# Kernel tuning notes

Measured on AMD Instinct MI355X. Metric: run time of the kernel, lower is better.

Reference implementation:

```python
import jax, jax.numpy as jnp
import numpy as np

N = 100000
E = 3200000
IN_C, H1, H2 = 512, 64, 32


def gcn_norm(edge_index, edge_weight, num_nodes):
    """PyG gcn_norm with add_self_loops=True: D^-1/2 (A+I) D^-1/2 edge weights."""
    row, col = edge_index[0], edge_index[1]
    loop = jnp.arange(num_nodes, dtype=edge_index.dtype)
    row = jnp.concatenate([row, loop])
    col = jnp.concatenate([col, loop])
    w = jnp.concatenate([edge_weight, jnp.ones((num_nodes,), edge_weight.dtype)])
    deg = jax.ops.segment_sum(w, col, num_segments=num_nodes)
    dinv = jnp.where(deg > 0, jax.lax.rsqrt(jnp.maximum(deg, 1e-12)), 0.0)
    wnorm = dinv[row] * w * dinv[col]
    return row, col, wnorm


def gcn_conv(x, W, b, row, col, wnorm, num_nodes):
    h = x @ W                                   # [N, out] linear first (out <= in)
    msg = wnorm[:, None] * h[row]               # gather + per-edge scale  [E+N, out]
    out = jax.ops.segment_sum(msg, col, num_segments=num_nodes)
    return out + b


def setup_inputs() -> dict:
    key = jax.random.key(0)
    ks = jax.random.split(key, 9)
    x = jax.random.normal(ks[0], (N, IN_C), dtype=jnp.float32)
    edge_index = jax.random.randint(ks[1], (2, E), 0, N, dtype=jnp.int64)
    edge_weight = jax.random.uniform(ks[2], (E,), dtype=jnp.float32)
    # Glorot-style init for GCN linear weights, zero bias (PyG defaults).
    def glorot(k, fan_in, fan_out):
        s = np.sqrt(6.0 / (fan_in + fan_out)).astype(np.float32)
        return jax.random.uniform(k, (fan_in, fan_out), jnp.float32, -s, s)
    return {
        "x": x,
        "edge_index": edge_index,
        "edge_weight": edge_weight,
        "W1": glorot(ks[3], IN_C, H1), "b1": jnp.zeros((H1,), jnp.float32),
        "W2": glorot(ks[4], H1, H2),  "b2": jnp.zeros((H2,), jnp.float32),
        "W3": glorot(ks[5], H2, 1),   "b3": jnp.zeros((1,), jnp.float32),
    }


def reference(x, edge_index, edge_weight, W1, b1, W2, b2, W3, b3):
    # Inference mode: dropout is identity (training=False).
    row, col, wnorm = gcn_norm(edge_index, edge_weight, N)  # cached=True: shared across layers
    h = jax.nn.relu(gcn_conv(x, W1, b1, row, col, wnorm, N))
    h = jax.nn.relu(gcn_conv(h, W2, b2, row, col, wnorm, N))
    h = gcn_conv(h, W3, b3, row, col, wnorm, N)
    return h.reshape(-1)  # [N]
```

## Files before the change

kernel.cpp:

```cpp
#include <hip/hip_runtime.h>

constexpr int BLK = 256;
constexpr int NBLKBIN = 512;
constexpr int MAXNB   = 1024;

typedef __bf16 bf16x8 __attribute__((ext_vector_type(8)));
typedef float  f32x4  __attribute__((ext_vector_type(4)));

__device__ __forceinline__ float blo(unsigned u) { return __uint_as_float(u << 16); }
__device__ __forceinline__ float bhi(unsigned u) { return __uint_as_float(u & 0xffff0000u); }

__global__ void k_detect(const int* __restrict__ ei, int e, int* __restrict__ flag) {
    if (blockIdx.x == 0 && threadIdx.x == 0) {
        int is64 = 1;
        for (int i = 0; i < 16; ++i)
            if (ei[2 * i + 1] != 0) { is64 = 0; break; }
        *flag = is64;
    }
}

__device__ __forceinline__ int load_idx(const void* ei, size_t pos, int is64) {
    if (is64) return (int)((const long long*)ei)[pos];
    return ((const int*)ei)[pos];
}

__global__ void k_zero_i(int* __restrict__ p, int n) {
    long i = (long)blockIdx.x * BLK + threadIdx.x;
    if (i < n) p[i] = 0;
}

__global__ __launch_bounds__(256) void k_binhist(const void* __restrict__ ei, int e,
                                                 const int* __restrict__ flag,
                                                 int* __restrict__ bucket_cnt, int nb) {
    __shared__ int hist[MAXNB];
    const int t = threadIdx.x;
    for (int b = t; b < nb; b += 256) hist[b] = 0;
    __syncthreads();
    const int is64 = *flag;
    const int chunk = (e + NBLKBIN - 1) / NBLKBIN;
    const int i0 = blockIdx.x * chunk;
    const int i1 = min(e, i0 + chunk);
    for (int i = i0 + t; i < i1; i += 256) {
        int dst = load_idx(ei, (size_t)e + i, is64);
        atomicAdd(&hist[dst >> 7], 1);
    }
    __syncthreads();
    for (int b = t; b < nb; b += 256) {
        int c = hist[b];
        if (c) atomicAdd(&bucket_cnt[b], c);
    }
}

__global__ void k_scanbkt(const int* __restrict__ cnt, int* __restrict__ offs,
                          int* __restrict__ cursor, int nb, int e) {
    __shared__ int sh[256];
    const int t = threadIdx.x;
    const int base = t * 4;
    int v[4]; int s = 0;
#pragma unroll
    for (int k = 0; k < 4; ++k) {
        int i = base + k;
        v[k] = (i < nb) ? cnt[i] : 0;
        s += v[k];
    }
    sh[t] = s;
    __syncthreads();
    for (int d = 1; d < 256; d <<= 1) {
        int x = (t >= d) ? sh[t - d] : 0;
        __syncthreads();
        sh[t] += x;
        __syncthreads();
    }
    int excl = (t == 0) ? 0 : sh[t - 1];
#pragma unroll
    for (int k = 0; k < 4; ++k) {
        int i = base + k;
        if (i < nb) { offs[i] = excl; cursor[i] = excl; excl += v[k]; }
    }
    if (t == 255) offs[nb] = e;
}

__global__ __launch_bounds__(256) void k_binscatter(const void* __restrict__ ei,
                                                    const float* __restrict__ ew, int e,
                                                    const int* __restrict__ flag,
                                                    int* __restrict__ bucket_cursor,
                                                    int2* __restrict__ binned, int nb) {
    __shared__ int hist[MAXNB];
    const int t = threadIdx.x;
    for (int b = t; b < nb; b += 256) hist[b] = 0;
    __syncthreads();
    const int is64 = *flag;
    const int chunk = (e + NBLKBIN - 1) / NBLKBIN;
    const int i0 = blockIdx.x * chunk;
    const int i1 = min(e, i0 + chunk);
    for (int i = i0 + t; i < i1; i += 256) {
        int dst = load_idx(ei, (size_t)e + i, is64);
        atomicAdd(&hist[dst >> 7], 1);
    }
    __syncthreads();
    for (int b = t; b < nb; b += 256) {
        int c = hist[b];
        int base = 0;
        if (c) base = atomicAdd(&bucket_cursor[b], c);
        hist[b] = base;
    }
    __syncthreads();
    for (int i = i0 + t; i < i1; i += 256) {
        int dst = load_idx(ei, (size_t)e + i, is64);
        int src = load_idx(ei, (size_t)i, is64);
        float w = ew[i];
        int bin = dst >> 7;
        int pos = atomicAdd(&hist[bin], 1);
        binned[pos] = make_int2(src | ((dst & 127) << 20), __float_as_int(w));
    }
}

__global__ __launch_bounds__(256) void k_bucketcnt(const int* __restrict__ bucket_offs,
                                                   const int2* __restrict__ binned,
                                                   int* __restrict__ counts,
                                                   float* __restrict__ dinv, int n) {
    __shared__ int   icnt[128];
    __shared__ float facc[128];
    const int t = threadIdx.x;
    const int k = blockIdx.x;
    if (t < 128) { icnt[t] = 0; facc[t] = 0.f; }
    __syncthreads();
    const int j0 = bucket_offs[k], j1 = bucket_offs[k + 1];
    for (int j = j0 + t; j < j1; j += 256) {
        int2 p = binned[j];
        int dl = ((unsigned)p.x) >> 20;
        atomicAdd(&icnt[dl], 1);
        atomicAdd(&facc[dl], __int_as_float(p.y));
    }
    __syncthreads();
    if (t < 128) {
        int nd = k * 128 + t;
        if (nd < n) {
            counts[nd] = icnt[t];
            dinv[nd] = rsqrtf(1.0f + facc[t]);
        }
    }
}

__global__ void k_scan1(const int* __restrict__ in, int* __restrict__ out,
                        int* __restrict__ bsum, int n) {
    __shared__ int sh[256];
    const int t = threadIdx.x;
    const int base = blockIdx.x * 1024 + t * 4;
    int v[4];
    int s = 0;
#pragma unroll
    for (int k = 0; k < 4; ++k) {
        int i = base + k;
        v[k] = (i < n) ? in[i] : 0;
        s += v[k];
    }
    sh[t] = s;
    __syncthreads();
    for (int d = 1; d < 256; d <<= 1) {
        int x = (t >= d) ? sh[t - d] : 0;
        __syncthreads();
        sh[t] += x;
        __syncthreads();
    }
    int excl = (t == 0) ? 0 : sh[t - 1];
    if (t == 255) bsum[blockIdx.x] = sh[255];
#pragma unroll
    for (int k = 0; k < 4; ++k) {
        int i = base + k;
        if (i < n) { out[i] = excl; excl += v[k]; }
    }
}

__global__ void k_scan2(int* __restrict__ bsum, int nb) {
    __shared__ int sh[128];
    const int t = threadIdx.x;
    sh[t] = (t < nb) ? bsum[t] : 0;
    __syncthreads();
    for (int d = 1; d < 128; d <<= 1) {
        int x = (t >= d) ? sh[t - d] : 0;
        __syncthreads();
        sh[t] += x;
        __syncthreads();
    }
    if (t < nb) bsum[t] = (t == 0) ? 0 : sh[t - 1];
}

__global__ void k_scan3(int* __restrict__ offs, const int* __restrict__ scanned,
                        const int* __restrict__ bsum, int n, int e) {
    long i = (long)blockIdx.x * BLK + threadIdx.x;
    if (i < n) offs[i] = scanned[i] + bsum[i >> 10];
    if (i == 0) offs[n] = e;
}

__global__ __launch_bounds__(256) void k_place(const int* __restrict__ bucket_offs,
                                               const int2* __restrict__ binned,
                                               const int* __restrict__ offs,
                                               const float* __restrict__ dinv,
                                               int2* __restrict__ csrp, int n) {
    __shared__ int cur[128];
    const int t = threadIdx.x;
    const int k = blockIdx.x;
    if (t < 128) {
        int nd = k * 128 + t;
        cur[t] = (nd < n) ? offs[nd] : 0;
    }
    __syncthreads();
    const int j0 = bucket_offs[k], j1 = bucket_offs[k + 1];
    for (int j = j0 + t; j < j1; j += 256) {
        int2 p = binned[j];
        int dl  = ((unsigned)p.x) >> 20;
        int src = p.x & 0xFFFFF;
        int pos = atomicAdd(&cur[dl], 1);
        float w2 = __int_as_float(p.y) * dinv[src];
        csrp[pos] = make_int2(src, __float_as_int(w2));
    }
}

__global__ void k_wcvt_frag(const float* __restrict__ W, __bf16* __restrict__ Wtf) {
    int i = blockIdx.x * BLK + threadIdx.x;
    if (i >= 4096) return;
    int lane = i & 63;
    int t    = (i >> 6) & 3;
    int k0c  = i >> 8;
    int col  = t * 16 + (lane & 15);
    int kbase = k0c * 32 + (lane >> 4) * 8;
    bf16x8 v;
#pragma unroll
    for (int j = 0; j < 8; ++j) v[j] = (__bf16)W[(size_t)(kbase + j) * 64 + col];
    *(bf16x8*)(Wtf + (size_t)i * 8) = v;
}

__global__ void k_wcvt_frag2(const float* __restrict__ W, __bf16* __restrict__ Wtf2) {
    int i = threadIdx.x;
    int lane = i & 63;
    int ct   = i >> 6;
    int t = ct & 1, chunk = ct >> 1;
    int col  = t * 16 + (lane & 15);
    int kbase = chunk * 32 + (lane >> 4) * 8;
    bf16x8 v;
#pragma unroll
    for (int j = 0; j < 8; ++j) v[j] = (__bf16)W[(size_t)(kbase + j) * 32 + col];
    *(bf16x8*)(Wtf2 + (size_t)i * 8) = v;
}

__global__ __launch_bounds__(256) void k_gemm1_mfma(const float* __restrict__ X,
                                                    const __bf16* __restrict__ Wtf,
                                                    __bf16* __restrict__ H, int nrows) {
    const int wave = threadIdx.x >> 6;
    const int lane = threadIdx.x & 63;
    const int l15  = lane & 15;
    const int lq   = lane >> 4;
    const long rbase = (long)blockIdx.x * 128 + wave * 32;

    long ar0 = rbase + l15;      if (ar0 >= nrows) ar0 = nrows - 1;
    long ar1 = rbase + 16 + l15; if (ar1 >= nrows) ar1 = nrows - 1;
    const float4* x0 = (const float4*)(X + (size_t)ar0 * 512) + lq * 2;
    const float4* x1 = (const float4*)(X + (size_t)ar1 * 512) + lq * 2;

    f32x4 acc[2][4];
#pragma unroll
    for (int r = 0; r < 2; ++r)
#pragma unroll
        for (int t = 0; t < 4; ++t) acc[r][t] = f32x4{0.f, 0.f, 0.f, 0.f};

    float4 pa[2][2][2];
#pragma unroll
    for (int s = 0; s < 2; ++s) {
        pa[s][0][0] = x0[s * 8]; pa[s][0][1] = x0[s * 8 + 1];
        pa[s][1][0] = x1[s * 8]; pa[s][1][1] = x1[s * 8 + 1];
    }

#pragma unroll
    for (int k0c = 0; k0c < 16; ++k0c) {
        const int s = k0c & 1;
        float4 a00 = pa[s][0][0], a01 = pa[s][0][1];
        float4 a10 = pa[s][1][0], a11 = pa[s][1][1];
        if (k0c + 2 < 16) {
            pa[s][0][0] = x0[(k0c + 2) * 8]; pa[s][0][1] = x0[(k0c + 2) * 8 + 1];
            pa[s][1][0] = x1[(k0c + 2) * 8]; pa[s][1][1] = x1[(k0c + 2) * 8 + 1];
        }
        bf16x8 af0, af1;
        af0[0] = (__bf16)a00.x; af0[1] = (__bf16)a00.y; af0[2] = (__bf16)a00.z; af0[3] = (__bf16)a00.w;
        af0[4] = (__bf16)a01.x; af0[5] = (__bf16)a01.y; af0[6] = (__bf16)a01.z; af0[7] = (__bf16)a01.w;
        af1[0] = (__bf16)a10.x; af1[1] = (__bf16)a10.y; af1[2] = (__bf16)a10.z; af1[3] = (__bf16)a10.w;
        af1[4] = (__bf16)a11.x; af1[5] = (__bf16)a11.y; af1[6] = (__bf16)a11.z; af1[7] = (__bf16)a11.w;
#pragma unroll
        for (int t = 0; t < 4; ++t) {
            bf16x8 bf_ = *(const bf16x8*)(Wtf + ((size_t)(k0c * 4 + t) * 64 + lane) * 8);
            acc[0][t] = __builtin_amdgcn_mfma_f32_16x16x32_bf16(af0, bf_, acc[0][t], 0, 0, 0);
            acc[1][t] = __builtin_amdgcn_mfma_f32_16x16x32_bf16(af1, bf_, acc[1][t], 0, 0, 0);
        }
    }
#pragma unroll
    for (int rr = 0; rr < 2; ++rr)
#pragma unroll
    for (int t = 0; t < 4; ++t)
#pragma unroll
    for (int r = 0; r < 4; ++r) {
        long row = rbase + rr * 16 + lq * 4 + r;
        if (row < nrows) H[(size_t)row * 64 + t * 16 + l15] = (__bf16)acc[rr][t][r];
    }
}

__global__ __launch_bounds__(256) void k_gemm2_mfma(const __bf16* __restrict__ A,
                                                    const __bf16* __restrict__ Wtf2,
                                                    __bf16* __restrict__ H, int nrows) {
    const int wave = threadIdx.x >> 6;
    const int lane = threadIdx.x & 63;
    const int l15  = lane & 15;
    const int lq   = lane >> 4;
    const long rbase = (long)blockIdx.x * 64 + wave * 16;

    long arow = rbase + l15;
    if (arow >= nrows) arow = nrows - 1;

    f32x4 acc[2] = {{0.f,0.f,0.f,0.f},{0.f,0.f,0.f,0.f}};
#pragma unroll
    for (int c = 0; c < 2; ++c) {
        bf16x8 af = *(const bf16x8*)(A + (size_t)arow * 64 + c * 32 + lq * 8);
#pragma unroll
        for (int t = 0; t < 2; ++t) {
            bf16x8 bf_ = *(const bf16x8*)(Wtf2 + ((size_t)(c * 2 + t) * 64 + lane) * 8);
            acc[t] = __builtin_amdgcn_mfma_f32_16x16x32_bf16(af, bf_, acc[t], 0, 0, 0);
        }
    }
#pragma unroll
    for (int t = 0; t < 2; ++t)
#pragma unroll
    for (int r = 0; r < 4; ++r) {
        long row = rbase + lq * 4 + r;
        if (row < nrows) H[(size_t)row * 32 + t * 16 + l15] = (__bf16)acc[t][r];
    }
}

template <int K, int EPI>
__global__ __launch_bounds__(256) void k_prop_bf(const int* __restrict__ offs,
                                                 const int2* __restrict__ csrp,
                                                 const __bf16* __restrict__ hb,
                                                 const float* __restrict__ dinv,
                                                 const float* __restrict__ bias,
                                                 const float* __restrict__ W3,
                                                 void* __restrict__ outv, int n) {
    constexpr int SUB = K / 2;
    constexpr int NPW = 64 / SUB;
    constexpr int NPB = 4 * NPW;
    const int t    = threadIdx.x;
    const int lane = t & 63;
    const int wave = t >> 6;
    const int chp  = lane & (SUB - 1);
    const int sub  = lane / SUB;
    const long nd  = (long)blockIdx.x * NPB + wave * NPW + sub;
    if (nd >= n) return;

    const unsigned short* h = (const unsigned short*)hb;
    const int j0 = offs[nd], j1 = offs[nd + 1];
    float a0 = 0.f, a1 = 0.f;
    int j = j0;
    for (; j + 3 < j1; j += 4) {
        int2 p0 = csrp[j];
        int2 p1 = csrp[j + 1];
        int2 p2 = csrp[j + 2];
        int2 p3 = csrp[j + 3];
        unsigned u0 = *(const unsigned*)(h + (size_t)p0.x * K + 2 * chp);
        unsigned u1 = *(const unsigned*)(h + (size_t)p1.x * K + 2 * chp);
        unsigned u2 = *(const unsigned*)(h + (size_t)p2.x * K + 2 * chp);
        unsigned u3 = *(const unsigned*)(h + (size_t)p3.x * K + 2 * chp);
        float w0 = __int_as_float(p0.y), w1 = __int_as_float(p1.y);
        float w2 = __int_as_float(p2.y), w3 = __int_as_float(p3.y);
        a0 = fmaf(w0, blo(u0), a0); a1 = fmaf(w0, bhi(u0), a1);
        a0 = fmaf(w1, blo(u1), a0); a1 = fmaf(w1, bhi(u1), a1);
        a0 = fmaf(w2, blo(u2), a0); a1 = fmaf(w2, bhi(u2), a1);
        a0 = fmaf(w3, blo(u3), a0); a1 = fmaf(w3, bhi(u3), a1);
    }
    for (; j < j1; ++j) {
        int2 p0 = csrp[j];
        unsigned u0 = *(const unsigned*)(h + (size_t)p0.x * K + 2 * chp);
        float w0 = __int_as_float(p0.y);
        a0 = fmaf(w0, blo(u0), a0);
        a1 = fmaf(w0, bhi(u0), a1);
    }
    const float di = dinv[nd];
    const float s  = di * di;
    unsigned us = *(const unsigned*)(h + (size_t)nd * K + 2 * chp);
    float2 bv = *(const float2*)(bias + 2 * chp);
    float o0 = fmaf(di, a0, fmaf(s, blo(us), bv.x));
    float o1 = fmaf(di, a1, fmaf(s, bhi(us), bv.y));
    o0 = fmaxf(o0, 0.f); o1 = fmaxf(o1, 0.f);
    if (EPI == 0) {
        unsigned short s0 = __builtin_bit_cast(unsigned short, (__bf16)o0);
        unsigned short s1 = __builtin_bit_cast(unsigned short, (__bf16)o1);
        ((unsigned*)outv)[(size_t)nd * SUB + chp] = (unsigned)s0 | ((unsigned)s1 << 16);
    } else {
        float2 wv = *(const float2*)(W3 + 2 * chp);
        float part = o0 * wv.x + o1 * wv.y;
#pragma unroll
        for (int d = SUB / 2; d >= 1; d >>= 1) part += __shfl_xor(part, d, SUB);
        if (chp == 0) ((float*)outv)[nd] = part;
    }
}

__global__ __launch_bounds__(256) void k_prop1(const int* __restrict__ offs,
                                               const int2* __restrict__ csrp,
                                               const float* __restrict__ h,
                                               const float* __restrict__ dinv,
                                               const float* __restrict__ bias,
                                               float* __restrict__ out, int n) {
    long nd = (long)blockIdx.x * BLK + threadIdx.x;
    if (nd >= n) return;
    const int j0 = offs[nd], j1 = offs[nd + 1];
    float acc = 0.f;
    int j = j0;
    for (; j + 3 < j1; j += 4) {
        int2 p0 = csrp[j];
        int2 p1 = csrp[j + 1];
        int2 p2 = csrp[j + 2];
        int2 p3 = csrp[j + 3];
        acc = fmaf(__int_as_float(p0.y), h[p0.x], acc);
        acc = fmaf(__int_as_float(p1.y), h[p1.x], acc);
        acc = fmaf(__int_as_float(p2.y), h[p2.x], acc);
        acc = fmaf(__int_as_float(p3.y), h[p3.x], acc);
    }
    for (; j < j1; ++j) {
        int2 p0 = csrp[j];
        acc = fmaf(__int_as_float(p0.y), h[p0.x], acc);
    }
    const float di = dinv[nd];
    out[nd] = fmaf(di, acc, fmaf(di * di, h[nd], bias[0]));
}

extern "C" void kernel_launch(void* const* d_in, const int* in_sizes, int n_in,
                              void* d_out, int out_size, void* d_ws, size_t ws_size,
                              hipStream_t stream) {
    const float* x  = (const float*)d_in[0];
    const void*  ei = d_in[1];
    const float* ew = (const float*)d_in[2];
    const float* W1 = (const float*)d_in[3];
    const float* b1 = (const float*)d_in[4];
    const float* W2 = (const float*)d_in[5];
    const float* b2 = (const float*)d_in[6];
    const float* W3 = (const float*)d_in[7];
    const float* b3 = (const float*)d_in[8];
    float* out = (float*)d_out;

    const int n = in_sizes[0] / 512;
    const int e = in_sizes[2];
    const int nb = (n + 127) >> 7;

    char* ws = (char*)d_ws;
    size_t off = 0;
    auto alloc = [&](size_t bytes) {
        void* p = ws + off;
        off = (off + bytes + 255) & ~(size_t)255;
        return p;
    };
    int*    flag     = (int*)   alloc(4);
    int2*   binned   = (int2*)  alloc((size_t)e * 8);
    __bf16* hbuf1    = (__bf16*)binned;
    int*    bkt_cnt  = (int*)   alloc((size_t)(MAXNB + 1) * 4);
    int*    bkt_offs = (int*)   alloc((size_t)(MAXNB + 1) * 4);
    int*    bkt_cur  = (int*)   alloc((size_t)(MAXNB + 1) * 4);
    int*    counts   = (int*)   alloc((size_t)n * 4);
    int*    offs     = (int*)   alloc((size_t)(n + 1) * 4);
    int*    bsum     = (int*)   alloc(512);
    int2*   csrp     = (int2*)  alloc((size_t)e * 8);
    float*  dinv     = (float*) alloc((size_t)n * 4);
    __bf16* pb64     = (__bf16*)alloc((size_t)n * 64 * 2);
    __bf16* hbuf2    = (__bf16*)alloc((size_t)n * 32 * 2);
    float*  h3       = (float*) alloc((size_t)n * 4);
    __bf16* Wtf      = (__bf16*)alloc((size_t)512 * 64 * 2);
    __bf16* Wtf2     = (__bf16*)alloc((size_t)64 * 32 * 2);
    (void)ws_size; (void)n_in; (void)out_size;

    const int gb_n = (n + BLK - 1) / BLK;
    const int nb_scan = (n + 1023) / 1024;

    k_detect<<<1, 64, 0, stream>>>((const int*)ei, e, flag);

    k_zero_i<<<(nb + BLK - 1) / BLK, BLK, 0, stream>>>(bkt_cnt, nb);
    k_binhist<<<NBLKBIN, 256, 0, stream>>>(ei, e, flag, bkt_cnt, nb);
    k_scanbkt<<<1, 256, 0, stream>>>(bkt_cnt, bkt_offs, bkt_cur, nb, e);
    k_binscatter<<<NBLKBIN, 256, 0, stream>>>(ei, ew, e, flag, bkt_cur, binned, nb);
    k_bucketcnt<<<nb, 256, 0, stream>>>(bkt_offs, binned, counts, dinv, n);
    k_scan1<<<nb_scan, 256, 0, stream>>>(counts, counts, bsum, n);
    k_scan2<<<1, 128, 0, stream>>>(bsum, nb_scan);
    k_scan3<<<gb_n, BLK, 0, stream>>>(offs, counts, bsum, n, e);
    k_place<<<nb, 256, 0, stream>>>(bkt_offs, binned, offs, dinv, csrp, n);

    k_wcvt_frag<<<(4096 + BLK - 1) / BLK, BLK, 0, stream>>>(W1, Wtf);
    k_wcvt_frag2<<<1, 256, 0, stream>>>(W2, Wtf2);

    k_gemm1_mfma<<<(n + 127) / 128, 256, 0, stream>>>(x, Wtf, hbuf1, n);
    k_prop_bf<64, 0><<<(n + 7) / 8, 256, 0, stream>>>(offs, csrp, hbuf1, dinv, b1, nullptr, pb64, n);

    k_gemm2_mfma<<<(n + 63) / 64, 256, 0, stream>>>(pb64, Wtf2, hbuf2, n);
    k_prop_bf<32, 1><<<(n + 15) / 16, 256, 0, stream>>>(offs, csrp, hbuf2, dinv, b2, W3, h3, n);

    k_prop1<<<gb_n, BLK, 0, stream>>>(offs, csrp, h3, dinv, b3, out, n);
}
```

Measured before the change: 384.6 us.

## Fuse prep kernels, inline index-width detection, widen propagation loads, fix-point degree

```diff
diff --git a/kernel.cpp b/kernel.cpp
--- a/kernel.cpp
+++ b/kernel.cpp
@@ -10,13 +10,13 @@
 __device__ __forceinline__ float blo(unsigned u) { return __uint_as_float(u << 16); }
 __device__ __forceinline__ float bhi(unsigned u) { return __uint_as_float(u & 0xffff0000u); }
 
-__global__ void k_detect(const int* __restrict__ ei, int e, int* __restrict__ flag) {
-    if (blockIdx.x == 0 && threadIdx.x == 0) {
-        int is64 = 1;
-        for (int i = 0; i < 16; ++i)
-            if (ei[2 * i + 1] != 0) { is64 = 0; break; }
-        *flag = is64;
-    }
+__device__ __forceinline__ int detect64(const void* ei) {
+    const int* p = (const int*)ei;
+    int is64 = 1;
+#pragma unroll
+    for (int i = 0; i < 16; ++i)
+        if (p[2 * i + 1] != 0) is64 = 0;
+    return is64;
 }
 
 __device__ __forceinline__ int load_idx(const void* ei, size_t pos, int is64) {
@@ -24,19 +24,45 @@
     return ((const int*)ei)[pos];
 }
 
-__global__ void k_zero_i(int* __restrict__ p, int n) {
-    long i = (long)blockIdx.x * BLK + threadIdx.x;
-    if (i < n) p[i] = 0;
+__global__ void k_prep(const float* __restrict__ W1, const float* __restrict__ W2,
+                       __bf16* __restrict__ Wtf, __bf16* __restrict__ Wtf2,
+                       int* __restrict__ bkt_cnt, int nb) {
+    const int b = blockIdx.x;
+    const int t = threadIdx.x;
+    if (b < 16) {
+        int i = b * 256 + t;
+        int lane = i & 63;
+        int tt   = (i >> 6) & 3;
+        int k0c  = i >> 8;
+        int col  = tt * 16 + (lane & 15);
+        int kbase = k0c * 32 + (lane >> 4) * 8;
+        bf16x8 v;
+#pragma unroll
+        for (int j = 0; j < 8; ++j) v[j] = (__bf16)W1[(size_t)(kbase + j) * 64 + col];
+        *(bf16x8*)(Wtf + (size_t)i * 8) = v;
+    } else if (b == 16) {
+        int i = t;
+        int lane = i & 63;
+        int ct   = i >> 6;
+        int tt = ct & 1, chunk = ct >> 1;
+        int col  = tt * 16 + (lane & 15);
+        int kbase = chunk * 32 + (lane >> 4) * 8;
+        bf16x8 v;
+#pragma unroll
+        for (int j = 0; j < 8; ++j) v[j] = (__bf16)W2[(size_t)(kbase + j) * 32 + col];
+        *(bf16x8*)(Wtf2 + (size_t)i * 8) = v;
+    } else {
+        for (int i = t; i < nb; i += 256) bkt_cnt[i] = 0;
+    }
 }
 
 __global__ __launch_bounds__(256) void k_binhist(const void* __restrict__ ei, int e,
-                                                 const int* __restrict__ flag,
                                                  int* __restrict__ bucket_cnt, int nb) {
     __shared__ int hist[MAXNB];
     const int t = threadIdx.x;
     for (int b = t; b < nb; b += 256) hist[b] = 0;
     __syncthreads();
-    const int is64 = *flag;
+    const int is64 = detect64(ei);
     const int chunk = (e + NBLKBIN - 1) / NBLKBIN;
     const int i0 = blockIdx.x * chunk;
     const int i1 = min(e, i0 + chunk);
@@ -82,14 +108,13 @@
 
 __global__ __launch_bounds__(256) void k_binscatter(const void* __restrict__ ei,
                                                     const float* __restrict__ ew, int e,
-                                                    const int* __restrict__ flag,
                                                     int* __restrict__ bucket_cursor,
                                                     int2* __restrict__ binned, int nb) {
     __shared__ int hist[MAXNB];
     const int t = threadIdx.x;
     for (int b = t; b < nb; b += 256) hist[b] = 0;
     __syncthreads();
-    const int is64 = *flag;
+    const int is64 = detect64(ei);
     const int chunk = (e + NBLKBIN - 1) / NBLKBIN;
     const int i0 = blockIdx.x * chunk;
     const int i1 = min(e, i0 + chunk);
@@ -119,25 +144,27 @@
                                                    const int2* __restrict__ binned,
                                                    int* __restrict__ counts,
                                                    float* __restrict__ dinv, int n) {
-    __shared__ int   icnt[128];
-    __shared__ float facc[128];
+    __shared__ int                icnt[128];
+    __shared__ unsigned long long facc[128];
     const int t = threadIdx.x;
     const int k = blockIdx.x;
-    if (t < 128) { icnt[t] = 0; facc[t] = 0.f; }
+    if (t < 128) { icnt[t] = 0; facc[t] = 0ull; }
     __syncthreads();
     const int j0 = bucket_offs[k], j1 = bucket_offs[k + 1];
+    const float SCALE = 1099511627776.f;
     for (int j = j0 + t; j < j1; j += 256) {
         int2 p = binned[j];
         int dl = ((unsigned)p.x) >> 20;
         atomicAdd(&icnt[dl], 1);
-        atomicAdd(&facc[dl], __int_as_float(p.y));
+        atomicAdd(&facc[dl], (unsigned long long)(__int_as_float(p.y) * SCALE));
     }
     __syncthreads();
     if (t < 128) {
         int nd = k * 128 + t;
         if (nd < n) {
             counts[nd] = icnt[t];
-            dinv[nd] = rsqrtf(1.0f + facc[t]);
+            float deg = fmaf((float)facc[t], 1.f / 1099511627776.f, 1.0f);
+            dinv[nd] = rsqrtf(deg);
         }
     }
 }
@@ -215,33 +242,6 @@
         float w2 = __int_as_float(p.y) * dinv[src];
         csrp[pos] = make_int2(src, __float_as_int(w2));
     }
-}
-
-__global__ void k_wcvt_frag(const float* __restrict__ W, __bf16* __restrict__ Wtf) {
-    int i = blockIdx.x * BLK + threadIdx.x;
-    if (i >= 4096) return;
-    int lane = i & 63;
-    int t    = (i >> 6) & 3;
-    int k0c  = i >> 8;
-    int col  = t * 16 + (lane & 15);
-    int kbase = k0c * 32 + (lane >> 4) * 8;
-    bf16x8 v;
-#pragma unroll
-    for (int j = 0; j < 8; ++j) v[j] = (__bf16)W[(size_t)(kbase + j) * 64 + col];
-    *(bf16x8*)(Wtf + (size_t)i * 8) = v;
-}
-
-__global__ void k_wcvt_frag2(const float* __restrict__ W, __bf16* __restrict__ Wtf2) {
-    int i = threadIdx.x;
-    int lane = i & 63;
-    int ct   = i >> 6;
-    int t = ct & 1, chunk = ct >> 1;
-    int col  = t * 16 + (lane & 15);
-    int kbase = chunk * 32 + (lane >> 4) * 8;
-    bf16x8 v;
-#pragma unroll
-    for (int j = 0; j < 8; ++j) v[j] = (__bf16)W[(size_t)(kbase + j) * 32 + col];
-    *(bf16x8*)(Wtf2 + (size_t)i * 8) = v;
 }
 
 __global__ __launch_bounds__(256) void k_gemm1_mfma(const float* __restrict__ X,
@@ -342,61 +342,72 @@
                                                  const float* __restrict__ bias,
                                                  const float* __restrict__ W3,
                                                  void* __restrict__ outv, int n) {
-    constexpr int SUB = K / 2;
+    constexpr int SUB = K / 4;
     constexpr int NPW = 64 / SUB;
     constexpr int NPB = 4 * NPW;
     const int t    = threadIdx.x;
     const int lane = t & 63;
     const int wave = t >> 6;
-    const int chp  = lane & (SUB - 1);
+    const int chq  = lane & (SUB - 1);
     const int sub  = lane / SUB;
     const long nd  = (long)blockIdx.x * NPB + wave * NPW + sub;
     if (nd >= n) return;
 
     const unsigned short* h = (const unsigned short*)hb;
     const int j0 = offs[nd], j1 = offs[nd + 1];
-    float a0 = 0.f, a1 = 0.f;
+    float a0 = 0.f, a1 = 0.f, a2 = 0.f, a3 = 0.f;
     int j = j0;
     for (; j + 3 < j1; j += 4) {
         int2 p0 = csrp[j];
         int2 p1 = csrp[j + 1];
         int2 p2 = csrp[j + 2];
         int2 p3 = csrp[j + 3];
-        unsigned u0 = *(const unsigned*)(h + (size_t)p0.x * K + 2 * chp);
-        unsigned u1 = *(const unsigned*)(h + (size_t)p1.x * K + 2 * chp);
-        unsigned u2 = *(const unsigned*)(h + (size_t)p2.x * K + 2 * chp);
-        unsigned u3 = *(const unsigned*)(h + (size_t)p3.x * K + 2 * chp);
+        uint2 u0 = *(const uint2*)(h + (size_t)p0.x * K + 4 * chq);
+        uint2 u1 = *(const uint2*)(h + (size_t)p1.x * K + 4 * chq);
+        uint2 u2 = *(const uint2*)(h + (size_t)p2.x * K + 4 * chq);
+        uint2 u3 = *(const uint2*)(h + (size_t)p3.x * K + 4 * chq);
         float w0 = __int_as_float(p0.y), w1 = __int_as_float(p1.y);
         float w2 = __int_as_float(p2.y), w3 = __int_as_float(p3.y);
-        a0 = fmaf(w0, blo(u0), a0); a1 = fmaf(w0, bhi(u0), a1);
-        a0 = fmaf(w1, blo(u1), a0); a1 = fmaf(w1, bhi(u1), a1);
-        a0 = fmaf(w2, blo(u2), a0); a1 = fmaf(w2, bhi(u2), a1);
-        a0 = fmaf(w3, blo(u3), a0); a1 = fmaf(w3, bhi(u3), a1);
+        a0 = fmaf(w0, blo(u0.x), a0); a1 = fmaf(w0, bhi(u0.x), a1);
+        a2 = fmaf(w0, blo(u0.y), a2); a3 = fmaf(w0, bhi(u0.y), a3);
+        a0 = fmaf(w1, blo(u1.x), a0); a1 = fmaf(w1, bhi(u1.x), a1);
+        a2 = fmaf(w1, blo(u1.y), a2); a3 = fmaf(w1, bhi(u1.y), a3);
+        a0 = fmaf(w2, blo(u2.x), a0); a1 = fmaf(w2, bhi(u2.x), a1);
+        a2 = fmaf(w2, blo(u2.y), a2); a3 = fmaf(w2, bhi(u2.y), a3);
+        a0 = fmaf(w3, blo(u3.x), a0); a1 = fmaf(w3, bhi(u3.x), a1);
+        a2 = fmaf(w3, blo(u3.y), a2); a3 = fmaf(w3, bhi(u3.y), a3);
     }
     for (; j < j1; ++j) {
         int2 p0 = csrp[j];
-        unsigned u0 = *(const unsigned*)(h + (size_t)p0.x * K + 2 * chp);
+        uint2 u0 = *(const uint2*)(h + (size_t)p0.x * K + 4 * chq);
         float w0 = __int_as_float(p0.y);
-        a0 = fmaf(w0, blo(u0), a0);
-        a1 = fmaf(w0, bhi(u0), a1);
+        a0 = fmaf(w0, blo(u0.x), a0); a1 = fmaf(w0, bhi(u0.x), a1);
+        a2 = fmaf(w0, blo(u0.y), a2); a3 = fmaf(w0, bhi(u0.y), a3);
     }
     const float di = dinv[nd];
     const float s  = di * di;
-    unsigned us = *(const unsigned*)(h + (size_t)nd * K + 2 * chp);
-    float2 bv = *(const float2*)(bias + 2 * chp);
-    float o0 = fmaf(di, a0, fmaf(s, blo(us), bv.x));
-    float o1 = fmaf(di, a1, fmaf(s, bhi(us), bv.y));
-    o0 = fmaxf(o0, 0.f); o1 = fmaxf(o1, 0.f);
+    uint2 us = *(const uint2*)(h + (size_t)nd * K + 4 * chq);
+    float4 bv = *(const float4*)(bias + 4 * chq);
+    float o0 = fmaf(di, a0, fmaf(s, blo(us.x), bv.x));
+    float o1 = fmaf(di, a1, fmaf(s, bhi(us.x), bv.y));
+    float o2 = fmaf(di, a2, fmaf(s, blo(us.y), bv.z));
+    float o3 = fmaf(di, a3, fmaf(s, bhi(us.y), bv.w));
+    o0 = fmaxf(o0, 0.f); o1 = fmaxf(o1, 0.f); o2 = fmaxf(o2, 0.f); o3 = fmaxf(o3, 0.f);
     if (EPI == 0) {
         unsigned short s0 = __builtin_bit_cast(unsigned short, (__bf16)o0);
         unsigned short s1 = __builtin_bit_cast(unsigned short, (__bf16)o1);
-        ((unsigned*)outv)[(size_t)nd * SUB + chp] = (unsigned)s0 | ((unsigned)s1 << 16);
+        unsigned short s2 = __builtin_bit_cast(unsigned short, (__bf16)o2);
+        unsigned short s3 = __builtin_bit_cast(unsigned short, (__bf16)o3);
+        uint2 pk;
+        pk.x = (unsigned)s0 | ((unsigned)s1 << 16);
+        pk.y = (unsigned)s2 | ((unsigned)s3 << 16);
+        *(uint2*)((unsigned*)outv + (size_t)nd * (K / 2) + 2 * chq) = pk;
     } else {
-        float2 wv = *(const float2*)(W3 + 2 * chp);
-        float part = o0 * wv.x + o1 * wv.y;
+        float4 wv = *(const float4*)(W3 + 4 * chq);
+        float part = o0 * wv.x + o1 * wv.y + o2 * wv.z + o3 * wv.w;
 #pragma unroll
         for (int d = SUB / 2; d >= 1; d >>= 1) part += __shfl_xor(part, d, SUB);
-        if (chp == 0) ((float*)outv)[nd] = part;
+        if (chq == 0) ((float*)outv)[nd] = part;
     }
 }
 
@@ -454,7 +465,6 @@
         off = (off + bytes + 255) & ~(size_t)255;
         return p;
     };
-    int*    flag     = (int*)   alloc(4);
     int2*   binned   = (int2*)  alloc((size_t)e * 8);
     __bf16* hbuf1    = (__bf16*)binned;
     int*    bkt_cnt  = (int*)   alloc((size_t)(MAXNB + 1) * 4);
@@ -475,26 +485,21 @@
     const int gb_n = (n + BLK - 1) / BLK;
     const int nb_scan = (n + 1023) / 1024;
 
-    k_detect<<<1, 64, 0, stream>>>((const int*)ei, e, flag);
-
-    k_zero_i<<<(nb + BLK - 1) / BLK, BLK, 0, stream>>>(bkt_cnt, nb);
-    k_binhist<<<NBLKBIN, 256, 0, stream>>>(ei, e, flag, bkt_cnt, nb);
+    k_prep<<<18, 256, 0, stream>>>(W1, W2, Wtf, Wtf2, bkt_cnt, nb);
+    k_binhist<<<NBLKBIN, 256, 0, stream>>>(ei, e, bkt_cnt, nb);
     k_scanbkt<<<1, 256, 0, stream>>>(bkt_cnt, bkt_offs, bkt_cur, nb, e);
-    k_binscatter<<<NBLKBIN, 256, 0, stream>>>(ei, ew, e, flag, bkt_cur, binned, nb);
+    k_binscatter<<<NBLKBIN, 256, 0, stream>>>(ei, ew, e, bkt_cur, binned, nb);
     k_bucketcnt<<<nb, 256, 0, stream>>>(bkt_offs, binned, counts, dinv, n);
     k_scan1<<<nb_scan, 256, 0, stream>>>(counts, counts, bsum, n);
     k_scan2<<<1, 128, 0, stream>>>(bsum, nb_scan);
     k_scan3<<<gb_n, BLK, 0, stream>>>(offs, counts, bsum, n, e);
     k_place<<<nb, 256, 0, stream>>>(bkt_offs, binned, offs, dinv, csrp, n);
 
-    k_wcvt_frag<<<(4096 + BLK - 1) / BLK, BLK, 0, stream>>>(W1, Wtf);
-    k_wcvt_frag2<<<1, 256, 0, stream>>>(W2, Wtf2);
-
     k_gemm1_mfma<<<(n + 127) / 128, 256, 0, stream>>>(x, Wtf, hbuf1, n);
-    k_prop_bf<64, 0><<<(n + 7) / 8, 256, 0, stream>>>(offs, csrp, hbuf1, dinv, b1, nullptr, pb64, n);
+    k_prop_bf<64, 0><<<(n + 15) / 16, 256, 0, stream>>>(offs, csrp, hbuf1, dinv, b1, nullptr, pb64, n);
 
     k_gemm2_mfma<<<(n + 63) / 64, 256, 0, stream>>>(pb64, Wtf2, hbuf2, n);
-    k_prop_bf<32, 1><<<(n + 15) / 16, 256, 0, stream>>>(offs, csrp, hbuf2, dinv, b2, W3, h3, n);
+    k_prop_bf<32, 1><<<(n + 31) / 32, 256, 0, stream>>>(offs, csrp, hbuf2, dinv, b2, W3, h3, n);
 
     k_prop1<<<gb_n, BLK, 0, stream>>>(offs, csrp, h3, dinv, b3, out, n);
 }
```

After: 349.0 us. 1.1x faster.
